# Kernel optimization log

Hardware: AMD Instinct MI355X
Metric: run time of the kernel (lower is better)

## Reference

```python
import jax, jax.numpy as jnp
import numpy as np

N = 200000   # nodes (Elliptic-scale)
E = 500000   # directed edges
F = 166      # in_channels / node feature dim
H = 128      # hidden_channels
C = 2        # out_channels
T = 49       # number of time steps


def setup_inputs() -> dict:
    key = jax.random.key(0)
    ks = jax.random.split(key, 12)
    x = jax.random.normal(ks[0], (N, F), jnp.float32)
    edge_index = jax.random.randint(ks[1], (2, E), 0, N, dtype=jnp.int32)
    time_step = jax.random.randint(ks[2], (N,), 0, T, dtype=jnp.int32)
    sF = 1.0 / np.sqrt(F)
    sH = 1.0 / np.sqrt(H)
    initial_w = jax.random.uniform(ks[3], (F, F), jnp.float32, -sF, sF)
    gru_w_ih = jax.random.uniform(ks[4], (3 * F, F), jnp.float32, -sF, sF)
    gru_w_hh = jax.random.uniform(ks[5], (3 * F, F), jnp.float32, -sF, sF)
    gru_b_ih = jax.random.uniform(ks[6], (3 * F,), jnp.float32, -sF, sF)
    gru_b_hh = jax.random.uniform(ks[7], (3 * F,), jnp.float32, -sF, sF)
    proj_w = jax.random.uniform(ks[8], (H, F), jnp.float32, -sF, sF)
    proj_b = jax.random.uniform(ks[9], (H,), jnp.float32, -sF, sF)
    cls_w = jax.random.uniform(ks[10], (C, H), jnp.float32, -sH, sH)
    cls_b = jax.random.uniform(ks[11], (C,), jnp.float32, -sH, sH)
    return {"x": x, "edge_index": edge_index, "time_step": time_step,
            "initial_w": initial_w, "gru_w_ih": gru_w_ih, "gru_w_hh": gru_w_hh,
            "gru_b_ih": gru_b_ih, "gru_b_hh": gru_b_hh,
            "proj_w": proj_w, "proj_b": proj_b, "cls_w": cls_w, "cls_b": cls_b}


def reference(x, edge_index, time_step, initial_w, gru_w_ih, gru_w_hh,
              gru_b_ih, gru_b_hh, proj_w, proj_b, cls_w, cls_b):
    src, dst = edge_index[0], edge_index[1]
    n = x.shape[0]

    def gru(W):
        # torch.nn.GRU single step, input = hidden = W  (FxF matrix, rows = batch)
        gi = W @ gru_w_ih.T + gru_b_ih
        gh = W @ gru_w_hh.T + gru_b_hh
        i_r, i_z, i_n = jnp.split(gi, 3, axis=-1)
        h_r, h_z, h_n = jnp.split(gh, 3, axis=-1)
        r = jax.nn.sigmoid(i_r + h_r)
        z = jax.nn.sigmoid(i_z + h_z)
        nn_ = jnp.tanh(i_n + r * h_n)
        return (1.0 - z) * nn_ + z * W

    def step(carry, t):
        W, logits = carry
        W = gru(W)  # evolve GCN weight (EvolveGCN-O)
        # subgraph of nodes with time_step <= t, expressed by masking (same math
        # as relabel+extract: inactive nodes contribute nothing, their outputs are ignored)
        act = time_step <= t
        ew = (act[src] & act[dst]).astype(x.dtype)
        # gcn_norm with self-loops: deg = in-degree over active edges + 1
        deg = jax.ops.segment_sum(ew, dst, num_segments=n) + 1.0
        dinv = jax.lax.rsqrt(deg)
        norm = ew * dinv[src] * dinv[dst]
        h = jnp.where(act[:, None], x, 0.0) @ W               # [N, F]
        agg = jax.ops.segment_sum(h[src] * norm[:, None], dst, num_segments=n)
        agg = agg + h / deg[:, None]                          # self-loop term dinv_i^2 * h_i
        z = jax.nn.relu(agg @ proj_w.T + proj_b)              # [N, H] (dropout: eval mode)
        lg = z @ cls_w.T + cls_b                              # [N, C]
        logits = jnp.where((time_step == t)[:, None], lg, logits)
        return (W, logits), None

    init = (initial_w, jnp.zeros((n, cls_w.shape[0]), x.dtype))
    (_, logits), _ = jax.lax.scan(step, init, jnp.arange(T, dtype=time_step.dtype))
    return logits
```

## Files before the change

### kernel.cpp

```cpp
#include <hip/hip_runtime.h>
#include <hip/hip_fp16.h>
#include <math.h>

#define NN 200000
#define NE 500000
#define FF 166
#define HH 128
#define CC 2
#define TT 49
#define GG 498
#define PADN 203136
#define MAXTILES 6400
#define KP 84
#define KPAD 192
#define SCB 512
#define SNB 391
#define HB 782

typedef _Float16 half2v __attribute__((ext_vector_type(2)));
typedef _Float16 f16x8 __attribute__((ext_vector_type(8)));
typedef float f32x4 __attribute__((ext_vector_type(4)));

static __device__ __forceinline__ float fdot2f(half2v a, half2v b, float c) {
#if __has_builtin(__builtin_amdgcn_fdot2)
    return __builtin_amdgcn_fdot2(a, b, c, false);
#else
    return c + (float)a.x * (float)b.x + (float)a.y * (float)b.y;
#endif
}

__global__ void prep_pack(const float* __restrict__ wih, const float* __restrict__ whh,
                          const float* __restrict__ projw,
                          _Float16* __restrict__ wkp, float* __restrict__ projwT) {
    int idx = blockIdx.x * 256 + threadIdx.x;
    const int A = 2 * KP * 512;
    if (idx < A) {
        int m = idx / (KP * 512);
        int r = idx - m * (KP * 512);
        int kp = r >> 9, c = r & 511;
        const float* Wm = m ? whh : wih;
        float x0 = 0.0f, x1 = 0.0f;
        if (c < GG) {
            int k0 = 2 * kp, k1 = 2 * kp + 1;
            if (k0 < FF) x0 = Wm[c * FF + k0];
            if (k1 < FF) x1 = Wm[c * FF + k1];
        }
        wkp[2 * idx]     = (_Float16)x0;
        wkp[2 * idx + 1] = (_Float16)x1;
    } else if (idx < A + FF * HH) {
        int q = idx - A;
        int k = q >> 7, h = q & 127;
        projwT[q] = projw[h * FF + k];
    }
}

__global__ __launch_bounds__(256) void x_to_h(const float* __restrict__ x, half2v* __restrict__ x2) {
    int idx = blockIdx.x * 256 + threadIdx.x;
    if (idx >= NN * 96) return;
    int row = idx / 96, cp = idx - row * 96;
    int c0 = cp * 2;
    float v0 = (c0 < FF) ? x[(size_t)row * FF + c0] : 0.0f;
    float v1 = (c0 + 1 < FF) ? x[(size_t)row * FF + c0 + 1] : 0.0f;
    half2v h;
    h[0] = (_Float16)v0;
    h[1] = (_Float16)v1;
    x2[idx] = h;
}

__global__ void count_indeg(const int* __restrict__ dst, int* __restrict__ off) {
    int e = blockIdx.x * 256 + threadIdx.x;
    if (e < NE) atomicAdd(&off[dst[e]], 1);
}

__global__ __launch_bounds__(256) void scan_p1(const int* __restrict__ off, int* __restrict__ bsum) {
    __shared__ int s[256];
    int b = blockIdx.x, tid = threadIdx.x;
    int i0 = b * SCB + tid * 2;
    int v = 0;
    if (i0 < NN) v += off[i0];
    if (i0 + 1 < NN) v += off[i0 + 1];
    s[tid] = v;
    __syncthreads();
    for (int d = 128; d > 0; d >>= 1) {
        if (tid < d) s[tid] += s[tid + d];
        __syncthreads();
    }
    if (tid == 0) bsum[b] = s[0];
}

__global__ __launch_bounds__(512) void scan_p2(const int* __restrict__ bsum, int* __restrict__ bpre,
                                               int* __restrict__ off) {
    __shared__ int s[512];
    int tid = threadIdx.x;
    int v = (tid < SNB) ? bsum[tid] : 0;
    s[tid] = v;
    __syncthreads();
    for (int d = 1; d < 512; d <<= 1) {
        int u = (tid >= d) ? s[tid - d] : 0;
        __syncthreads();
        s[tid] += u;
        __syncthreads();
    }
    bpre[tid] = s[tid] - v;
    if (tid == 511) off[NN] = s[511];
}

__global__ __launch_bounds__(512) void scan_p3(int* __restrict__ off, const int* __restrict__ bpre) {
    __shared__ int s[512];
    int b = blockIdx.x, tid = threadIdx.x;
    int i = b * SCB + tid;
    int v = (i < NN) ? off[i] : 0;
    s[tid] = v;
    __syncthreads();
    for (int d = 1; d < 512; d <<= 1) {
        int u = (tid >= d) ? s[tid - d] : 0;
        __syncthreads();
        s[tid] += u;
        __syncthreads();
    }
    if (i < NN) off[i] = s[tid] - v + bpre[b];
}

__global__ void fill_adj(const int* __restrict__ src, const int* __restrict__ dst,
                         const int* __restrict__ ts,
                         const int* __restrict__ off, int* __restrict__ cursor,
                         int* __restrict__ adjsrc, int* __restrict__ dstid,
                         int* __restrict__ tsrc) {
    int e = blockIdx.x * 256 + threadIdx.x;
    if (e < NE) {
        int d = dst[e];
        int s = src[e];
        int p = atomicAdd(&cursor[d], 1);
        int pos = off[d] + p;
        adjsrc[pos] = s;
        dstid[pos] = d;
        tsrc[pos] = ts[s];
    }
}

__global__ __launch_bounds__(256) void degf_hist(const int* __restrict__ off, const int* __restrict__ tsrc,
                                                 const int* __restrict__ ts, _Float16* __restrict__ dinvh,
                                                 float* __restrict__ selfdeg) {
    __shared__ unsigned short sh[TT * 256];
    int tid = threadIdx.x;
    int i = blockIdx.x * 256 + tid;
    for (int t = 0; t < TT; ++t) sh[t * 256 + tid] = 0;
    if (i >= NN) return;
    int tsi = ts[i];
    int e0 = off[i], e1 = off[i + 1];
    for (int e = e0; e < e1; ++e) {
        int tj = tsrc[e];
        sh[tj * 256 + tid]++;
    }
    int cum = 1;
    for (int t = 0; t < TT; ++t) {
        cum += sh[t * 256 + tid];
        dinvh[(size_t)t * NN + i] = (_Float16)rsqrtf((float)cum);
        if (t == tsi) selfdeg[i] = 1.0f / (float)cum;
    }
}

__global__ __launch_bounds__(256) void edge_prep(const int* __restrict__ adjsrc, const int* __restrict__ dstid,
                                                 const int* __restrict__ tsrc,
                                                 const int* __restrict__ ts, const _Float16* __restrict__ dinvh,
                                                 int2* __restrict__ ewp) {
    int e = blockIdx.x * 256 + threadIdx.x;
    if (e >= NE) return;
    int j = adjsrc[e], i = dstid[e];
    int t = ts[i];
    float w = 0.0f;
    if (tsrc[e] <= t)
        w = (float)dinvh[(size_t)t * NN + j] * (float)dinvh[(size_t)t * NN + i];
    int2 p;
    p.x = j;
    p.y = __float_as_int(w);
    ewp[e] = p;
}

__global__ __launch_bounds__(256) void hist_rank(const int* __restrict__ ts,
                                                 int* __restrict__ cnt, int* __restrict__ rank) {
    __shared__ int h[TT];
    int tid = threadIdx.x, b = blockIdx.x;
    if (tid < TT) h[tid] = 0;
    __syncthreads();
    int i = b * 256 + tid;
    if (i < NN) {
        int t = ts[i];
        rank[i] = atomicAdd(&h[t], 1);
    }
    __syncthreads();
    if (tid < TT) cnt[b * TT + tid] = h[tid];
}

__global__ __launch_bounds__(256) void bucket_scan(const int* __restrict__ cnt,
                                                   int* __restrict__ basecol, int* __restrict__ bcnt) {
    __shared__ int s[256];
    int t = blockIdx.x, tid = threadIdx.x;
    const int CH = (HB + 255) / 256;
    int b0 = tid * CH;
    int loc[CH];
    int sum = 0;
    for (int u = 0; u < CH; ++u) {
        int b = b0 + u;
        int v = (b < HB) ? cnt[b * TT + t] : 0;
        loc[u] = sum;
        sum += v;
    }
    s[tid] = sum;
    __syncthreads();
    for (int d = 1; d < 256; d <<= 1) {
        int u = (tid >= d) ? s[tid - d] : 0;
        __syncthreads();
        s[tid] += u;
        __syncthreads();
    }
    int base = s[tid] - sum;
    for (int u = 0; u < CH; ++u) {
        int b = b0 + u;
        if (b < HB) basecol[b * TT + t] = base + loc[u];
    }
    if (tid == 255) bcnt[t] = s[255];
}

__global__ __launch_bounds__(256) void perm_scatter(const int* __restrict__ ts, const int* __restrict__ rank,
                                                    const int* __restrict__ basecol, const int* __restrict__ pstart,
                                                    int* __restrict__ perm) {
    int b = blockIdx.x;
    int i = b * 256 + threadIdx.x;
    if (i < NN) {
        int t = ts[i];
        perm[pstart[t] + basecol[b * TT + t] + rank[i]] = i;
    }
}

__global__ void make_tiles(const int* __restrict__ bcnt, int* __restrict__ pstart,
                           int* __restrict__ tile_t, int* __restrict__ tile_r0,
                           int* __restrict__ meta) {
    __shared__ int s_nt[64];
    int t = threadIdx.x;
    int nt = (t < TT) ? (bcnt[t] + 31) / 32 : 0;
    s_nt[t] = nt;
    __syncthreads();
    for (int d = 1; d < 64; d <<= 1) {
        int v = (t >= d) ? s_nt[t - d] : 0;
        __syncthreads();
        s_nt[t] += v;
        __syncthreads();
    }
    int ntbase = s_nt[t] - nt;
    int pbase = ntbase * 32;
    if (t < TT) {
        pstart[t] = pbase;
        for (int u = 0; u < nt; ++u) {
            tile_t[ntbase + u] = t;
            tile_r0[ntbase + u] = pbase + u * 32;
        }
    }
    if (t == 63) {
        meta[0] = s_nt[63];
        meta[1] = s_nt[63] * 32;
        pstart[TT] = s_nt[63] * 32;
    }
}

__global__ __launch_bounds__(512) void gru_evolve(
        const float* __restrict__ initial_w,
        const _Float16* __restrict__ wkp,
        const float* __restrict__ bih, const float* __restrict__ bhh,
        float* __restrict__ W_all) {
    __shared__ float s_w[FF];
    __shared__ __align__(16) _Float16 s_wh[2 * KP];
    __shared__ float s_pre[2][512];
    int tid = threadIdx.x;
    int row = blockIdx.x;

    if (tid < FF) {
        float v = initial_w[(size_t)row * FF + tid];
        s_w[tid] = v;
        s_wh[tid] = (_Float16)v;
    } else if (tid < 2 * KP) {
        s_wh[tid] = (_Float16)0.0f;
    }

    int cc0 = tid * 2;
    bool act = cc0 < 996;
    int m = (cc0 >= 498) ? 1 : 0;
    int c0 = act ? (cc0 - m * 498) : 0;

    half2v wr0[KP], wr1[KP];
    {
        const half2v* __restrict__ pW =
            (const half2v*)wkp + (size_t)(act ? m : 0) * (KP * 512) + c0;
        #pragma unroll
        for (int kp = 0; kp < KP; ++kp) {
            wr0[kp] = pW[(size_t)(kp << 9)];
            wr1[kp] = pW[(size_t)(kp << 9) + 1];
        }
    }

    float bi_r = 0, bi_z = 0, bi_n = 0, bh_r = 0, bh_z = 0, bh_n = 0;
    if (tid < FF) {
        bi_r = bih[tid]; bi_z = bih[FF + tid]; bi_n = bih[2 * FF + tid];
        bh_r = bhh[tid]; bh_z = bhh[FF + tid]; bh_n = bhh[2 * FF + tid];
    }
    __syncthreads();

    const f16x8* s_wh8 = (const f16x8*)s_wh;
    for (int t = 0; t < TT; ++t) {
        if (act) {
            float a0 = 0.0f, a1 = 0.0f;
            #pragma unroll
            for (int q = 0; q < 21; ++q) {
                f16x8 w8 = s_wh8[q];
                half2v h0 = __builtin_shufflevector(w8, w8, 0, 1);
                half2v h1 = __builtin_shufflevector(w8, w8, 2, 3);
                half2v h2 = __builtin_shufflevector(w8, w8, 4, 5);
                half2v h3 = __builtin_shufflevector(w8, w8, 6, 7);
                a0 = fdot2f(wr0[4 * q + 0], h0, a0);  a1 = fdot2f(wr1[4 * q + 0], h0, a1);
                a0 = fdot2f(wr0[4 * q + 1], h1, a0);  a1 = fdot2f(wr1[4 * q + 1], h1, a1);
                a0 = fdot2f(wr0[4 * q + 2], h2, a0);  a1 = fdot2f(wr1[4 * q + 2], h2, a1);
                a0 = fdot2f(wr0[4 * q + 3], h3, a0);  a1 = fdot2f(wr1[4 * q + 3], h3, a1);
            }
            s_pre[m][c0]     = a0;
            s_pre[m][c0 + 1] = a1;
        }
        __syncthreads();
        if (tid < FF) {
            float i_r = s_pre[0][tid]          + bi_r;
            float h_r = s_pre[1][tid]          + bh_r;
            float i_z = s_pre[0][FF + tid]     + bi_z;
            float h_z = s_pre[1][FF + tid]     + bh_z;
            float i_n = s_pre[0][2 * FF + tid] + bi_n;
            float h_n = s_pre[1][2 * FF + tid] + bh_n;
            float rg = 1.0f / (1.0f + expf(-(i_r + h_r)));
            float zg = 1.0f / (1.0f + expf(-(i_z + h_z)));
            float ng = tanhf(i_n + rg * h_n);
            float wnew = (1.0f - zg) * ng + zg * s_w[tid];
            s_w[tid] = wnew;
            s_wh[tid] = (_Float16)wnew;
            W_all[((size_t)t * FF + row) * FF + tid] = wnew;
        }
        __syncthreads();
    }
}

__global__ __launch_bounds__(1024) void m_build(const float* __restrict__ W_all,
                                                const float* __restrict__ projwT,
                                                _Float16* __restrict__ Mh) {
    __shared__ __align__(16) float sw[8][168];
    int blk = blockIdx.x;
    int t = blk / 24, rb = blk - t * 24;
    int tid = threadIdx.x;
    int r0 = rb * 8;
    for (int idx = tid; idx < 8 * FF; idx += 1024) {
        int rr = idx / FF, k = idx - rr * FF;
        int r = r0 + rr;
        sw[rr][k] = (r < FF) ? W_all[((size_t)t * FF + r) * FF + k] : 0.0f;
    }
    __syncthreads();
    int rr = tid >> 7, h = tid & 127;
    int r = r0 + rr;
    if (r >= KPAD) return;
    float acc = 0.0f;
    if (r < FF) {
        const float* __restrict__ pw = projwT + h;
        #pragma unroll 4
        for (int c4 = 0; c4 < 164; c4 += 4) {
            float4 w = *(const float4*)&sw[rr][c4];
            acc += w.x * pw[(size_t)(c4 + 0) << 7];
            acc += w.y * pw[(size_t)(c4 + 1) << 7];
            acc += w.z * pw[(size_t)(c4 + 2) << 7];
            acc += w.w * pw[(size_t)(c4 + 3) << 7];
        }
        acc += sw[rr][164] * pw[(size_t)164 << 7];
        acc += sw[rr][165] * pw[(size_t)165 << 7];
    }
    Mh[((size_t)t * HH + h) * KPAD + r] = (_Float16)acc;
}

__global__ __launch_bounds__(512) void gemm_fused3(
        const int* __restrict__ meta, const int* __restrict__ tile_t,
        const int* __restrict__ tile_r0, const int* __restrict__ perm,
        const float* __restrict__ selfdeg, const half2v* __restrict__ x2,
        const int* __restrict__ off, const int2* __restrict__ ewp,
        const _Float16* __restrict__ Mh, const float* __restrict__ proj_b,
        const float* __restrict__ cls_w, const float* __restrict__ cls_b,
        float* __restrict__ out) {
    __shared__ __align__(16) char smraw[32 * 130 * 4];
    _Float16* sY = (_Float16*)smraw;
    float* sP = (float*)smraw;
    int bid = blockIdx.x;
    if (bid >= meta[0]) return;
    int t = tile_t[bid], r0 = tile_r0[bid];
    int tid = threadIdx.x;
    int lane = tid & 63;
    int w = tid >> 6;
    bool lo = lane < 32;

    int rbase = w * 4;
    int idx4[4], ep[4], ee[4];
    float ax[4], ay[4], bx[4], by[4];
    #pragma unroll
    for (int q = 0; q < 4; ++q) {
        int i = perm[r0 + rbase + q];
        idx4[q] = i;
        ax[q] = ay[q] = bx[q] = by[q] = 0.0f;
        ep[q] = 0; ee[q] = 0;
        if (i >= 0) { ep[q] = off[i]; ee[q] = off[i + 1]; }
    }
    #pragma unroll
    for (int q = 0; q < 4; ++q) {
        int i = idx4[q];
        if (i >= 0) {
            float sw = selfdeg[i];
            const half2v* xi = x2 + (size_t)i * 96;
            half2v h0 = xi[lane];
            ax[q] = sw * (float)h0[0];
            ay[q] = sw * (float)h0[1];
            if (lo) {
                half2v h1 = xi[64 + lane];
                bx[q] = sw * (float)h1[0];
                by[q] = sw * (float)h1[1];
            }
        }
    }
    while ((ep[0] < ee[0]) | (ep[1] < ee[1]) | (ep[2] < ee[2]) | (ep[3] < ee[3])) {
        float wv[4]; int js[4];
        #pragma unroll
        for (int q = 0; q < 4; ++q) {
            wv[q] = 0.0f; js[q] = 0;
            if (ep[q] < ee[q]) {
                int2 p = ewp[ep[q]++];
                js[q] = p.x;
                wv[q] = __int_as_float(p.y);
            }
        }
        #pragma unroll
        for (int q = 0; q < 4; ++q) {
            if (wv[q] != 0.0f) {
                const half2v* xj = x2 + (size_t)js[q] * 96;
                half2v g0 = xj[lane];
                ax[q] += wv[q] * (float)g0[0];
                ay[q] += wv[q] * (float)g0[1];
                if (lo) {
                    half2v g1 = xj[64 + lane];
                    bx[q] += wv[q] * (float)g1[0];
                    by[q] += wv[q] * (float)g1[1];
                }
            }
        }
    }
    #pragma unroll
    for (int q = 0; q < 4; ++q) {
        half2v o0;
        o0[0] = (_Float16)ax[q];
        o0[1] = (_Float16)ay[q];
        *(half2v*)(sY + (rbase + q) * 200 + lane * 2) = o0;
        if (lo) {
            half2v o1;
            o1[0] = (_Float16)bx[q];
            o1[1] = (_Float16)by[q];
            *(half2v*)(sY + (rbase + q) * 200 + 128 + lane * 2) = o1;
        }
    }
    __syncthreads();

    int lr = lane & 15;
    int kg = lane >> 4;
    int c0 = w * 16;
    f32x4 acc0 = {0, 0, 0, 0}, acc1 = {0, 0, 0, 0};
    const _Float16* B0 = Mh + ((size_t)t * HH + c0 + lr) * KPAD + kg * 8;
    const _Float16* A0 = sY + lr * 200 + kg * 8;
    const _Float16* A1 = A0 + 16 * 200;

    #pragma unroll
    for (int s = 0; s < 6; ++s) {
        f16x8 b0 = *(const f16x8*)(B0 + s * 32);
        f16x8 a0 = *(const f16x8*)(A0 + s * 32);
        f16x8 a1 = *(const f16x8*)(A1 + s * 32);
        acc0 = __builtin_amdgcn_mfma_f32_16x16x32_f16(a0, b0, acc0, 0, 0, 0);
        acc1 = __builtin_amdgcn_mfma_f32_16x16x32_f16(a1, b0, acc1, 0, 0, 0);
    }

    float pb = proj_b[c0 + lr];
    __syncthreads();
    int prow = kg * 4;
    int colw = c0 + lr;
    #pragma unroll
    for (int r = 0; r < 4; ++r) {
        sP[(prow + r) * 130 + colw]      = fmaxf(acc0[r] + pb, 0.0f);
        sP[(16 + prow + r) * 130 + colw] = fmaxf(acc1[r] + pb, 0.0f);
    }
    __syncthreads();

    int row = tid >> 4, cc = (tid >> 3) & 1, qq = tid & 7;
    const float* pr = sP + row * 130 + qq * 16;
    const float* cw = cls_w + cc * HH + qq * 16;
    float s = 0.0f;
    #pragma unroll
    for (int h = 0; h < 16; ++h) s += pr[h] * cw[h];
    s += __shfl_xor(s, 1);
    s += __shfl_xor(s, 2);
    s += __shfl_xor(s, 4);
    if (qq == 0) {
        int node = perm[r0 + row];
        if (node >= 0) out[(size_t)node * CC + cc] = s + cls_b[cc];
    }
}

extern "C" void kernel_launch(void* const* d_in, const int* in_sizes, int n_in,
                              void* d_out, int out_size, void* d_ws, size_t ws_size,
                              hipStream_t stream) {
    const float* x = (const float*)d_in[0];
    const int* ei = (const int*)d_in[1];
    const int* srcp = ei;
    const int* dstp = ei + NE;
    const int* ts = (const int*)d_in[2];
    const float* initial_w = (const float*)d_in[3];
    const float* wih = (const float*)d_in[4];
    const float* whh = (const float*)d_in[5];
    const float* bih = (const float*)d_in[6];
    const float* bhh = (const float*)d_in[7];
    const float* projw = (const float*)d_in[8];
    const float* projb = (const float*)d_in[9];
    const float* clsw = (const float*)d_in[10];
    const float* clsb = (const float*)d_in[11];
    float* out = (float*)d_out;

    char* base = (char*)d_ws;
    size_t o = 0;
    auto alloc = [&](size_t bytes) { size_t r = o; o = (o + bytes + 255) & ~(size_t)255; return r; };

    float*    W_all   = (float*)   (base + alloc((size_t)TT * FF * FF * 4));
    _Float16* Mh      = (_Float16*)(base + alloc((size_t)TT * HH * KPAD * 2));
    _Float16* wkp     = (_Float16*)(base + alloc((size_t)2 * KP * 512 * 2 * 2));
    float*    projwT  = (float*)   (base + alloc((size_t)FF * HH * 4));
    int*      off     = (int*)     (base + alloc((size_t)(NN + 1) * 4));
    int*      cursor  = (int*)     (base + alloc((size_t)NN * 4));
    int*      adjsrc  = (int*)     (base + alloc((size_t)NE * 4));
    int*      dstid   = (int*)     (base + alloc((size_t)NE * 4));
    int*      tsrc    = (int*)     (base + alloc((size_t)NE * 4));
    int2*     ewp     = (int2*)    (base + alloc((size_t)NE * 8));
    _Float16* dinvh   = (_Float16*)(base + alloc((size_t)TT * NN * 2));
    float*    selfdeg = (float*)   (base + alloc((size_t)NN * 4));
    int*      bcnt    = (int*)     (base + alloc((size_t)TT * 4));
    int*      pstart  = (int*)     (base + alloc((size_t)(TT + 1) * 4));
    int*      meta    = (int*)     (base + alloc(2 * 4));
    int*      tile_t  = (int*)     (base + alloc((size_t)MAXTILES * 4));
    int*      tile_r0 = (int*)     (base + alloc((size_t)MAXTILES * 4));
    int*      perm    = (int*)     (base + alloc((size_t)PADN * 4));
    int*      bsum    = (int*)     (base + alloc((size_t)512 * 4));
    int*      bpre    = (int*)     (base + alloc((size_t)520 * 4));
    int*      cnt     = (int*)     (base + alloc((size_t)HB * TT * 4));
    int*      basecol = (int*)     (base + alloc((size_t)HB * TT * 4));
    int*      rank    = (int*)     (base + alloc((size_t)NN * 4));
    half2v*   x2      = (half2v*)  (base + alloc((size_t)NN * 96 * 4));

    hipMemsetAsync(off, 0, (size_t)(NN + 1) * 4, stream);
    hipMemsetAsync(cursor, 0, (size_t)NN * 4, stream);
    hipMemsetAsync(perm, 0xFF, (size_t)PADN * 4, stream);

    prep_pack<<<420, 256, 0, stream>>>(wih, whh, projw, wkp, projwT);
    x_to_h<<<(NN * 96 + 255) / 256, 256, 0, stream>>>(x, x2);
    count_indeg<<<(NE + 255) / 256, 256, 0, stream>>>(dstp, off);
    hist_rank<<<HB, 256, 0, stream>>>(ts, cnt, rank);
    scan_p1<<<SNB, 256, 0, stream>>>(off, bsum);
    scan_p2<<<1, 512, 0, stream>>>(bsum, bpre, off);
    scan_p3<<<SNB, 512, 0, stream>>>(off, bpre);
    fill_adj<<<(NE + 255) / 256, 256, 0, stream>>>(srcp, dstp, ts, off, cursor, adjsrc, dstid, tsrc);
    degf_hist<<<(NN + 255) / 256, 256, 0, stream>>>(off, tsrc, ts, dinvh, selfdeg);
    edge_prep<<<(NE + 255) / 256, 256, 0, stream>>>(adjsrc, dstid, tsrc, ts, dinvh, ewp);
    bucket_scan<<<TT, 256, 0, stream>>>(cnt, basecol, bcnt);
    make_tiles<<<1, 64, 0, stream>>>(bcnt, pstart, tile_t, tile_r0, meta);
    perm_scatter<<<HB, 256, 0, stream>>>(ts, rank, basecol, pstart, perm);

    gru_evolve<<<FF, 512, 0, stream>>>(initial_w, wkp, bih, bhh, W_all);
    m_build<<<TT * 24, 1024, 0, stream>>>(W_all, projwT, Mh);

    gemm_fused3<<<MAXTILES, 512, 0, stream>>>(meta, tile_t, tile_r0, perm, selfdeg,
                                              x2, off, ewp, Mh, projb, clsw, clsb, out);
}
```

Measured before the change: 391.1 us.

## Permute fp16 features into tile order and compact active edges per node

Node features are now scattered into the time-bucketed permutation order, so each tile's own rows can be loaded contiguously into shared memory with wide vector loads. The per-edge prep is replaced by a per-node compaction that drops inactive edges, stores permuted source indices, and records an active count, so the gather loop skips zero-weight edges entirely. The dstid array is removed. The tradeoff is a serial per-node compaction loop with poor parallelism on high-degree nodes, plus a random-write scatter of x.

```diff
diff --git a/kernel.cpp b/kernel.cpp
--- a/kernel.cpp
+++ b/kernel.cpp
@@ -54,17 +54,19 @@
     }
 }
 
-__global__ __launch_bounds__(256) void x_to_h(const float* __restrict__ x, half2v* __restrict__ x2) {
+__global__ __launch_bounds__(256) void x_scatter_h(const float* __restrict__ x,
+                                                   const int* __restrict__ pos,
+                                                   half2v* __restrict__ x2p) {
     int idx = blockIdx.x * 256 + threadIdx.x;
     if (idx >= NN * 96) return;
-    int row = idx / 96, cp = idx - row * 96;
+    int i = idx / 96, cp = idx - i * 96;
     int c0 = cp * 2;
-    float v0 = (c0 < FF) ? x[(size_t)row * FF + c0] : 0.0f;
-    float v1 = (c0 + 1 < FF) ? x[(size_t)row * FF + c0 + 1] : 0.0f;
+    float v0 = (c0 < FF) ? x[(size_t)i * FF + c0] : 0.0f;
+    float v1 = (c0 + 1 < FF) ? x[(size_t)i * FF + c0 + 1] : 0.0f;
     half2v h;
     h[0] = (_Float16)v0;
     h[1] = (_Float16)v1;
-    x2[idx] = h;
+    x2p[(size_t)pos[i] * 96 + cp] = h;
 }
 
 __global__ void count_indeg(const int* __restrict__ dst, int* __restrict__ off) {
@@ -124,8 +126,7 @@
 __global__ void fill_adj(const int* __restrict__ src, const int* __restrict__ dst,
                          const int* __restrict__ ts,
                          const int* __restrict__ off, int* __restrict__ cursor,
-                         int* __restrict__ adjsrc, int* __restrict__ dstid,
-                         int* __restrict__ tsrc) {
+                         int* __restrict__ adjsrc, int* __restrict__ tsrc) {
     int e = blockIdx.x * 256 + threadIdx.x;
     if (e < NE) {
         int d = dst[e];
@@ -133,7 +134,6 @@
         int p = atomicAdd(&cursor[d], 1);
         int pos = off[d] + p;
         adjsrc[pos] = s;
-        dstid[pos] = d;
         tsrc[pos] = ts[s];
     }
 }
@@ -160,21 +160,28 @@
     }
 }
 
-__global__ __launch_bounds__(256) void edge_prep(const int* __restrict__ adjsrc, const int* __restrict__ dstid,
-                                                 const int* __restrict__ tsrc,
-                                                 const int* __restrict__ ts, const _Float16* __restrict__ dinvh,
-                                                 int2* __restrict__ ewp) {
-    int e = blockIdx.x * 256 + threadIdx.x;
-    if (e >= NE) return;
-    int j = adjsrc[e], i = dstid[e];
+__global__ __launch_bounds__(256) void edge_compact(
+        const int* __restrict__ off, const int* __restrict__ adjsrc, const int* __restrict__ tsrc,
+        const int* __restrict__ ts, const _Float16* __restrict__ dinvh, const int* __restrict__ pos,
+        int2* __restrict__ ewp, int* __restrict__ nact) {
+    int i = blockIdx.x * 256 + threadIdx.x;
+    if (i >= NN) return;
     int t = ts[i];
-    float w = 0.0f;
-    if (tsrc[e] <= t)
-        w = (float)dinvh[(size_t)t * NN + j] * (float)dinvh[(size_t)t * NN + i];
-    int2 p;
-    p.x = j;
-    p.y = __float_as_int(w);
-    ewp[e] = p;
+    const _Float16* dv = dinvh + (size_t)t * NN;
+    float dvi = (float)dv[i];
+    int e0 = off[i], e1 = off[i + 1];
+    int c = e0;
+    for (int e = e0; e < e1; ++e) {
+        if (tsrc[e] <= t) {
+            int j = adjsrc[e];
+            float w = (float)dv[j] * dvi;
+            int2 p;
+            p.x = pos[j];
+            p.y = __float_as_int(w);
+            ewp[c++] = p;
+        }
+    }
+    nact[i] = c - e0;
 }
 
 __global__ __launch_bounds__(256) void hist_rank(const int* __restrict__ ts,
@@ -224,12 +231,14 @@
 
 __global__ __launch_bounds__(256) void perm_scatter(const int* __restrict__ ts, const int* __restrict__ rank,
                                                     const int* __restrict__ basecol, const int* __restrict__ pstart,
-                                                    int* __restrict__ perm) {
+                                                    int* __restrict__ perm, int* __restrict__ pos) {
     int b = blockIdx.x;
     int i = b * 256 + threadIdx.x;
     if (i < NN) {
         int t = ts[i];
-        perm[pstart[t] + basecol[b * TT + t] + rank[i]] = i;
+        int p = pstart[t] + basecol[b * TT + t] + rank[i];
+        perm[p] = i;
+        pos[i] = p;
     }
 }
 
@@ -378,11 +387,12 @@
     Mh[((size_t)t * HH + h) * KPAD + r] = (_Float16)acc;
 }
 
-__global__ __launch_bounds__(512) void gemm_fused3(
+__global__ __launch_bounds__(512) void gemm_fused4(
         const int* __restrict__ meta, const int* __restrict__ tile_t,
         const int* __restrict__ tile_r0, const int* __restrict__ perm,
-        const float* __restrict__ selfdeg, const half2v* __restrict__ x2,
-        const int* __restrict__ off, const int2* __restrict__ ewp,
+        const float* __restrict__ selfdeg, const half2v* __restrict__ x2p,
+        const int* __restrict__ off, const int* __restrict__ nact,
+        const int2* __restrict__ ewp,
         const _Float16* __restrict__ Mh, const float* __restrict__ proj_b,
         const float* __restrict__ cls_w, const float* __restrict__ cls_b,
         float* __restrict__ out) {
@@ -397,31 +407,42 @@
     int w = tid >> 6;
     bool lo = lane < 32;
 
+    {
+        const uint4* src = (const uint4*)(x2p + (size_t)r0 * 96);
+        #pragma unroll
+        for (int u = 0; u < 2; ++u) {
+            int q = tid + u * 512;
+            if (q < 768) {
+                int row = q / 24, kc = q - row * 24;
+                *(uint4*)(sY + row * 200 + kc * 8) = src[q];
+            }
+        }
+    }
+    __syncthreads();
+
     int rbase = w * 4;
-    int idx4[4], ep[4], ee[4];
+    int ep[4], ee[4];
     float ax[4], ay[4], bx[4], by[4];
     #pragma unroll
     for (int q = 0; q < 4; ++q) {
-        int i = perm[r0 + rbase + q];
-        idx4[q] = i;
-        ax[q] = ay[q] = bx[q] = by[q] = 0.0f;
+        int r = rbase + q;
+        int i = perm[r0 + r];
+        float sw = 0.0f;
         ep[q] = 0; ee[q] = 0;
-        if (i >= 0) { ep[q] = off[i]; ee[q] = off[i + 1]; }
-    }
-    #pragma unroll
-    for (int q = 0; q < 4; ++q) {
-        int i = idx4[q];
         if (i >= 0) {
-            float sw = selfdeg[i];
-            const half2v* xi = x2 + (size_t)i * 96;
-            half2v h0 = xi[lane];
-            ax[q] = sw * (float)h0[0];
-            ay[q] = sw * (float)h0[1];
-            if (lo) {
-                half2v h1 = xi[64 + lane];
-                bx[q] = sw * (float)h1[0];
-                by[q] = sw * (float)h1[1];
-            }
+            sw = selfdeg[i];
+            int e0 = off[i];
+            ep[q] = e0;
+            ee[q] = e0 + nact[i];
+        }
+        half2v h0 = *(const half2v*)(sY + r * 200 + lane * 2);
+        ax[q] = sw * (float)h0[0];
+        ay[q] = sw * (float)h0[1];
+        bx[q] = 0.0f; by[q] = 0.0f;
+        if (lo) {
+            half2v h1 = *(const half2v*)(sY + r * 200 + 128 + lane * 2);
+            bx[q] = sw * (float)h1[0];
+            by[q] = sw * (float)h1[1];
         }
     }
     while ((ep[0] < ee[0]) | (ep[1] < ee[1]) | (ep[2] < ee[2]) | (ep[3] < ee[3])) {
@@ -438,7 +459,7 @@
         #pragma unroll
         for (int q = 0; q < 4; ++q) {
             if (wv[q] != 0.0f) {
-                const half2v* xj = x2 + (size_t)js[q] * 96;
+                const half2v* xj = x2p + (size_t)js[q] * 96;
                 half2v g0 = xj[lane];
                 ax[q] += wv[q] * (float)g0[0];
                 ay[q] += wv[q] * (float)g0[1];
@@ -450,6 +471,7 @@
             }
         }
     }
+    __syncthreads();
     #pragma unroll
     for (int q = 0; q < 4; ++q) {
         half2v o0;
@@ -538,11 +560,12 @@
     int*      off     = (int*)     (base + alloc((size_t)(NN + 1) * 4));
     int*      cursor  = (int*)     (base + alloc((size_t)NN * 4));
     int*      adjsrc  = (int*)     (base + alloc((size_t)NE * 4));
-    int*      dstid   = (int*)     (base + alloc((size_t)NE * 4));
     int*      tsrc    = (int*)     (base + alloc((size_t)NE * 4));
     int2*     ewp     = (int2*)    (base + alloc((size_t)NE * 8));
     _Float16* dinvh   = (_Float16*)(base + alloc((size_t)TT * NN * 2));
     float*    selfdeg = (float*)   (base + alloc((size_t)NN * 4));
+    int*      nact    = (int*)     (base + alloc((size_t)NN * 4));
+    int*      pos     = (int*)     (base + alloc((size_t)NN * 4));
     int*      bcnt    = (int*)     (base + alloc((size_t)TT * 4));
     int*      pstart  = (int*)     (base + alloc((size_t)(TT + 1) * 4));
     int*      meta    = (int*)     (base + alloc(2 * 4));
@@ -554,29 +577,29 @@
     int*      cnt     = (int*)     (base + alloc((size_t)HB * TT * 4));
     int*      basecol = (int*)     (base + alloc((size_t)HB * TT * 4));
     int*      rank    = (int*)     (base + alloc((size_t)NN * 4));
-    half2v*   x2      = (half2v*)  (base + alloc((size_t)NN * 96 * 4));
+    half2v*   x2p     = (half2v*)  (base + alloc((size_t)PADN * 96 * 4));
 
     hipMemsetAsync(off, 0, (size_t)(NN + 1) * 4, stream);
     hipMemsetAsync(cursor, 0, (size_t)NN * 4, stream);
     hipMemsetAsync(perm, 0xFF, (size_t)PADN * 4, stream);
 
     prep_pack<<<420, 256, 0, stream>>>(wih, whh, projw, wkp, projwT);
-    x_to_h<<<(NN * 96 + 255) / 256, 256, 0, stream>>>(x, x2);
     count_indeg<<<(NE + 255) / 256, 256, 0, stream>>>(dstp, off);
     hist_rank<<<HB, 256, 0, stream>>>(ts, cnt, rank);
     scan_p1<<<SNB, 256, 0, stream>>>(off, bsum);
     scan_p2<<<1, 512, 0, stream>>>(bsum, bpre, off);
     scan_p3<<<SNB, 512, 0, stream>>>(off, bpre);
-    fill_adj<<<(NE + 255) / 256, 256, 0, stream>>>(srcp, dstp, ts, off, cursor, adjsrc, dstid, tsrc);
+    fill_adj<<<(NE + 255) / 256, 256, 0, stream>>>(srcp, dstp, ts, off, cursor, adjsrc, tsrc);
     degf_hist<<<(NN + 255) / 256, 256, 0, stream>>>(off, tsrc, ts, dinvh, selfdeg);
-    edge_prep<<<(NE + 255) / 256, 256, 0, stream>>>(adjsrc, dstid, tsrc, ts, dinvh, ewp);
     bucket_scan<<<TT, 256, 0, stream>>>(cnt, basecol, bcnt);
     make_tiles<<<1, 64, 0, stream>>>(bcnt, pstart, tile_t, tile_r0, meta);
-    perm_scatter<<<HB, 256, 0, stream>>>(ts, rank, basecol, pstart, perm);
+    perm_scatter<<<HB, 256, 0, stream>>>(ts, rank, basecol, pstart, perm, pos);
+    x_scatter_h<<<(NN * 96 + 255) / 256, 256, 0, stream>>>(x, pos, x2p);
+    edge_compact<<<(NN + 255) / 256, 256, 0, stream>>>(off, adjsrc, tsrc, ts, dinvh, pos, ewp, nact);
 
     gru_evolve<<<FF, 512, 0, stream>>>(initial_w, wkp, bih, bhh, W_all);
     m_build<<<TT * 24, 1024, 0, stream>>>(W_all, projwT, Mh);
 
-    gemm_fused3<<<MAXTILES, 512, 0, stream>>>(meta, tile_t, tile_r0, perm, selfdeg,
-                                              x2, off, ewp, Mh, projb, clsw, clsb, out);
-}
+    gemm_fused4<<<MAXTILES, 512, 0, stream>>>(meta, tile_t, tile_r0, perm, selfdeg,
+                                              x2p, off, nact, ewp, Mh, projb, clsw, clsb, out);
+}
```

After: 379.2 us. 3.0% less time.
